# Kernel optimization log

Hardware: AMD Instinct MI355X
Metric: run time of the kernel (lower is better)

## Reference

```python
import jax, jax.numpy as jnp
import numpy as np

N_NODES = 20000
DEG = 32
N_EDGES = N_NODES * DEG
NUM_USERS = 100000
D = 128


def setup_inputs() -> dict:
    key = jax.random.key(0)
    ks = jax.random.split(key, 10)
    nodes = jax.random.randint(ks[0], (N_NODES,), 0, NUM_USERS)
    neigh_idx = jax.random.randint(ks[1], (N_EDGES,), 0, NUM_USERS)
    # fixed-degree flattening of the ragged to_neighs lists: every node has DEG neighbors
    seg_ids = jnp.repeat(jnp.arange(N_NODES), DEG)
    u2e = jax.random.normal(ks[2], (NUM_USERS, D), dtype=jnp.float32)
    W1 = jax.random.normal(ks[3], (2 * D, D), dtype=jnp.float32) * 0.05
    b1 = jax.random.normal(ks[4], (D,), dtype=jnp.float32) * 0.05
    W2 = jax.random.normal(ks[5], (D, D), dtype=jnp.float32) * 0.05
    b2 = jax.random.normal(ks[6], (D,), dtype=jnp.float32) * 0.05
    w3 = jax.random.normal(ks[7], (D, 1), dtype=jnp.float32) * 0.05
    b3 = jax.random.normal(ks[8], (1,), dtype=jnp.float32) * 0.05
    return {"nodes": nodes, "neigh_idx": neigh_idx, "seg_ids": seg_ids,
            "u2e": u2e, "W1": W1, "b1": b1, "W2": W2, "b2": b2, "w3": w3, "b3": b3}


def reference(nodes, neigh_idx, seg_ids, u2e, W1, b1, W2, b2, w3, b3):
    n = nodes.shape[0]
    e_u = u2e[neigh_idx]                 # [E, D] neighbor embeddings
    u_rep = u2e[nodes][seg_ids]          # [E, D] center-node embedding repeated per neighbor
    x = jnp.concatenate([e_u, u_rep], axis=1)        # [E, 2D]
    h = jax.nn.relu(x @ W1 + b1)                      # [E, D]
    h = jax.nn.relu(h @ W2 + b2)                      # [E, D]
    s = (h @ w3 + b3)[:, 0]                           # [E] attention logits
    # segment softmax over each node's neighbor set
    smax = jax.ops.segment_max(s, seg_ids, num_segments=n)
    e = jnp.exp(s - smax[seg_ids])
    denom = jax.ops.segment_sum(e, seg_ids, num_segments=n)
    att = e / denom[seg_ids]                          # [E]
    # attention-weighted neighbor sum (e_u^T @ att per node)
    out = jax.ops.segment_sum(att[:, None] * e_u, seg_ids, num_segments=n)  # [N, D]
    return out
```

## Files before the change

kernel.cpp:

```cpp
#include <hip/hip_runtime.h>
#include <hip/hip_bf16.h>

#define DD 128
#define DEG 32

typedef __attribute__((ext_vector_type(8))) _Float16 half8;
typedef __attribute__((ext_vector_type(4))) float f32x4;

__device__ __forceinline__ unsigned pkh(float a, float b) {
    _Float16 ha = (_Float16)a, hb = (_Float16)b;
    return (unsigned)__builtin_bit_cast(unsigned short, ha)
         | ((unsigned)__builtin_bit_cast(unsigned short, hb) << 16);
}
__device__ __forceinline__ float h2f_lo(unsigned u) {
    return (float)__builtin_bit_cast(_Float16, (unsigned short)(u & 0xffff));
}
__device__ __forceinline__ float h2f_hi(unsigned u) {
    return (float)__builtin_bit_cast(_Float16, (unsigned short)(u >> 16));
}

__global__ __launch_bounds__(256) void k_prep(
    const float* __restrict__ W1, const float* __restrict__ W2,
    uint4* __restrict__ w1img, uint4* __restrict__ w2t)
{
    int t = blockIdx.x * 256 + threadIdx.x;
    if (t < 4096) {
        int l = t & 63, f = t >> 6, k4 = f & 3, nt = f >> 2;
        int n = nt * 16 + (l & 15), kb = k4 * 32 + ((l >> 4) & 3) * 8;
        float v[8];
        #pragma unroll
        for (int i = 0; i < 8; ++i) {
            int k = kb + i;
            v[i] = (n < DD) ? W1[k * DD + n] : W1[(DD + k) * DD + (n - DD)];
        }
        uint4 r;
        r.x = pkh(v[0], v[1]); r.y = pkh(v[2], v[3]);
        r.z = pkh(v[4], v[5]); r.w = pkh(v[6], v[7]);
        w1img[t] = r;
    } else if (t < 6144) {
        int q = t - 4096;
        int l = q & 63, f = q >> 6, k4 = f & 3, mt = f >> 2;
        int ch = mt * 16 + (l & 15), kb = k4 * 32 + ((l >> 4) & 3) * 8;
        float v[8];
        #pragma unroll
        for (int i = 0; i < 8; ++i) v[i] = W2[(kb + i) * DD + ch];
        uint4 r;
        r.x = pkh(v[0], v[1]); r.y = pkh(v[2], v[3]);
        r.z = pkh(v[4], v[5]); r.w = pkh(v[6], v[7]);
        w2t[q] = r;
    }
}

__global__ __launch_bounds__(256) void k_cast(
    const float4* __restrict__ u2e4, uint4* __restrict__ ub16v, int total8)
{
    int i = blockIdx.x * 256 + threadIdx.x;
    if (i >= total8) return;
    float4 v0 = u2e4[(size_t)i * 2], v1 = u2e4[(size_t)i * 2 + 1];
    uint4 r;
    r.x = pkh(v0.x, v0.y); r.y = pkh(v0.z, v0.w);
    r.z = pkh(v1.x, v1.y); r.w = pkh(v1.z, v1.w);
    ub16v[i] = r;
}

__global__ __launch_bounds__(256) void k_qn(
    const int* __restrict__ nodes, const float* __restrict__ u2e,
    const uint4* __restrict__ w1img, const float* __restrict__ b1,
    unsigned short* __restrict__ Qnh, int n)
{
    const int t = threadIdx.x, w = t >> 6, l = t & 63;
    const int base = blockIdx.x * 128;

    half8 a[2][4];
    #pragma unroll
    for (int nt = 0; nt < 2; ++nt) {
        int row = min(base + w * 32 + nt * 16 + (l & 15), n - 1);
        int user = nodes[row];
        const float* rp = u2e + (size_t)user * DD + ((l >> 4) << 3);
        #pragma unroll
        for (int k4 = 0; k4 < 4; ++k4) {
            float4 v0 = *reinterpret_cast<const float4*>(rp + k4 * 32);
            float4 v1 = *reinterpret_cast<const float4*>(rp + k4 * 32 + 4);
            uint4 r;
            r.x = pkh(v0.x, v0.y); r.y = pkh(v0.z, v0.w);
            r.z = pkh(v1.x, v1.y); r.w = pkh(v1.z, v1.w);
            a[nt][k4] = __builtin_bit_cast(half8, r);
        }
    }
    const int chq = (l >> 4) << 2;
    #pragma unroll
    for (int mt = 0; mt < 8; ++mt) {
        half8 wf[4];
        #pragma unroll
        for (int k4 = 0; k4 < 4; ++k4)
            wf[k4] = __builtin_bit_cast(half8, w1img[((8 + mt) * 4 + k4) * 64 + l]);
        float4 b1v = *reinterpret_cast<const float4*>(&b1[mt * 16 + chq]);
        #pragma unroll
        for (int nt = 0; nt < 2; ++nt) {
            f32x4 acc = {0.f, 0.f, 0.f, 0.f};
            #pragma unroll
            for (int k4 = 0; k4 < 4; ++k4)
                acc = __builtin_amdgcn_mfma_f32_16x16x32_f16(wf[k4], a[nt][k4], acc, 0, 0, 0);
            int row = base + w * 32 + nt * 16 + (l & 15);
            if (row < n) {
                uint2 pk;
                pk.x = pkh(acc[0] + b1v.x, acc[1] + b1v.y);
                pk.y = pkh(acc[2] + b1v.z, acc[3] + b1v.w);
                *reinterpret_cast<uint2*>(&Qnh[(size_t)row * DD + mt * 16 + chq]) = pk;
            }
        }
    }
}

__global__ __launch_bounds__(512, 4) void k_node(
    const int* __restrict__ neigh, const _Float16* __restrict__ ub16,
    const unsigned short* __restrict__ Qnh, const uint4* __restrict__ w1img,
    const uint4* __restrict__ w2t, const float* __restrict__ b2,
    const float* __restrict__ w3, float4* __restrict__ out4, int n)
{
    __shared__ uint4 s_img[4096];

    const int t = threadIdx.x, w = t >> 6, l = t & 63;
    const int node = min(blockIdx.x * 8 + w, n - 1);
    const int g = l >> 4, c = l & 15;

    #pragma unroll
    for (int i = 0; i < 4; ++i) s_img[i * 512 + t] = w1img[i * 512 + t];
    #pragma unroll
    for (int i = 0; i < 4; ++i) s_img[2048 + i * 512 + t] = w2t[i * 512 + t];

    const int idx0 = neigh[node * DEG + c];
    const int idx1 = neigh[node * DEG + 16 + c];
    const int koff = g * 8;
    half8 ub0[4], ub1[4];
    #pragma unroll
    for (int k4 = 0; k4 < 4; ++k4)
        ub0[k4] = *reinterpret_cast<const half8*>(&ub16[(size_t)idx0 * DD + k4 * 32 + koff]);
    #pragma unroll
    for (int k4 = 0; k4 < 4; ++k4)
        ub1[k4] = *reinterpret_cast<const half8*>(&ub16[(size_t)idx1 * DD + k4 * 32 + koff]);
    uint2 qnh[8];
    #pragma unroll
    for (int mt = 0; mt < 8; ++mt)
        qnh[mt] = *reinterpret_cast<const uint2*>(&Qnh[(size_t)node * DD + mt * 16 + g * 4]);

    __syncthreads();

    uint2 hp0[8], hp1[8];
    #pragma unroll
    for (int mt = 0; mt < 8; ++mt) {
        half8 wf[4];
        #pragma unroll
        for (int k4 = 0; k4 < 4; ++k4)
            wf[k4] = __builtin_bit_cast(half8, s_img[(mt * 4 + k4) * 64 + l]);
        f32x4 a0 = {0.f, 0.f, 0.f, 0.f}, a1 = {0.f, 0.f, 0.f, 0.f};
        #pragma unroll
        for (int k4 = 0; k4 < 4; ++k4)
            a0 = __builtin_amdgcn_mfma_f32_16x16x32_f16(wf[k4], ub0[k4], a0, 0, 0, 0);
        #pragma unroll
        for (int k4 = 0; k4 < 4; ++k4)
            a1 = __builtin_amdgcn_mfma_f32_16x16x32_f16(wf[k4], ub1[k4], a1, 0, 0, 0);
        float q0 = h2f_lo(qnh[mt].x), q1 = h2f_hi(qnh[mt].x);
        float q2 = h2f_lo(qnh[mt].y), q3 = h2f_hi(qnh[mt].y);
        hp0[mt].x = pkh(fmaxf(a0[0] + q0, 0.f), fmaxf(a0[1] + q1, 0.f));
        hp0[mt].y = pkh(fmaxf(a0[2] + q2, 0.f), fmaxf(a0[3] + q3, 0.f));
        hp1[mt].x = pkh(fmaxf(a1[0] + q0, 0.f), fmaxf(a1[1] + q1, 0.f));
        hp1[mt].y = pkh(fmaxf(a1[2] + q2, 0.f), fmaxf(a1[3] + q3, 0.f));
    }

    const int srcA = ((g & 1) << 5) + c;
    const int hiSel = g >> 1;
    half8 hb0[4], hb1[4];
    #pragma unroll
    for (int k4 = 0; k4 < 4; ++k4) {
        unsigned d[4], e[4];
        #pragma unroll
        for (int j = 0; j < 4; ++j) {
            int src = srcA + ((j >> 1) << 4);
            unsigned vE = (unsigned)__shfl((int)((j & 1) ? hp0[2 * k4].y : hp0[2 * k4].x), src);
            unsigned vO = (unsigned)__shfl((int)((j & 1) ? hp0[2 * k4 + 1].y : hp0[2 * k4 + 1].x), src);
            d[j] = hiSel ? vO : vE;
            unsigned uE = (unsigned)__shfl((int)((j & 1) ? hp1[2 * k4].y : hp1[2 * k4].x), src);
            unsigned uO = (unsigned)__shfl((int)((j & 1) ? hp1[2 * k4 + 1].y : hp1[2 * k4 + 1].x), src);
            e[j] = hiSel ? uO : uE;
        }
        uint4 du = {d[0], d[1], d[2], d[3]};
        uint4 eu = {e[0], e[1], e[2], e[3]};
        hb0[k4] = __builtin_bit_cast(half8, du);
        hb1[k4] = __builtin_bit_cast(half8, eu);
    }

    float pl0 = 0.f, pl1 = 0.f;
    #pragma unroll
    for (int mt = 0; mt < 8; ++mt) {
        half8 wf[4];
        #pragma unroll
        for (int k4 = 0; k4 < 4; ++k4)
            wf[k4] = __builtin_bit_cast(half8, s_img[2048 + (mt * 4 + k4) * 64 + l]);
        float4 b2v = *reinterpret_cast<const float4*>(&b2[mt * 16 + g * 4]);
        float4 w3v = *reinterpret_cast<const float4*>(&w3[mt * 16 + g * 4]);
        f32x4 a0 = {0.f, 0.f, 0.f, 0.f}, a1 = {0.f, 0.f, 0.f, 0.f};
        #pragma unroll
        for (int k4 = 0; k4 < 4; ++k4)
            a0 = __builtin_amdgcn_mfma_f32_16x16x32_f16(wf[k4], hb0[k4], a0, 0, 0, 0);
        #pragma unroll
        for (int k4 = 0; k4 < 4; ++k4)
            a1 = __builtin_amdgcn_mfma_f32_16x16x32_f16(wf[k4], hb1[k4], a1, 0, 0, 0);
        pl0 += fmaxf(a0[0] + b2v.x, 0.f) * w3v.x + fmaxf(a0[1] + b2v.y, 0.f) * w3v.y
             + fmaxf(a0[2] + b2v.z, 0.f) * w3v.z + fmaxf(a0[3] + b2v.w, 0.f) * w3v.w;
        pl1 += fmaxf(a1[0] + b2v.x, 0.f) * w3v.x + fmaxf(a1[1] + b2v.y, 0.f) * w3v.y
             + fmaxf(a1[2] + b2v.z, 0.f) * w3v.z + fmaxf(a1[3] + b2v.w, 0.f) * w3v.w;
    }
    pl0 += __shfl_xor(pl0, 16); pl0 += __shfl_xor(pl0, 32);
    pl1 += __shfl_xor(pl1, 16); pl1 += __shfl_xor(pl1, 32);

    float mx = fmaxf(pl0, pl1);
    #pragma unroll
    for (int mask = 1; mask <= 8; mask <<= 1) mx = fmaxf(mx, __shfl_xor(mx, mask));
    float e0 = __expf(pl0 - mx), e1 = __expf(pl1 - mx);
    float sm = e0 + e1;
    #pragma unroll
    for (int mask = 1; mask <= 8; mask <<= 1) sm += __shfl_xor(sm, mask);
    float inv = __frcp_rn(sm);
    float att0 = e0 * inv, att1 = e1 * inv;

    float o[4][8];
    #pragma unroll
    for (int k4 = 0; k4 < 4; ++k4)
        #pragma unroll
        for (int i = 0; i < 8; ++i)
            o[k4][i] = att0 * (float)ub0[k4][i] + att1 * (float)ub1[k4][i];
    #pragma unroll
    for (int mask = 1; mask <= 8; mask <<= 1) {
        #pragma unroll
        for (int k4 = 0; k4 < 4; ++k4)
            #pragma unroll
            for (int i = 0; i < 8; ++i)
                o[k4][i] += __shfl_xor(o[k4][i], mask);
    }
    if (c == 0) {
        #pragma unroll
        for (int k4 = 0; k4 < 4; ++k4) {
            float4 r0 = make_float4(o[k4][0], o[k4][1], o[k4][2], o[k4][3]);
            float4 r1 = make_float4(o[k4][4], o[k4][5], o[k4][6], o[k4][7]);
            out4[(size_t)node * 32 + k4 * 8 + g * 2]     = r0;
            out4[(size_t)node * 32 + k4 * 8 + g * 2 + 1] = r1;
        }
    }
}

extern "C" void kernel_launch(void* const* d_in, const int* in_sizes, int n_in,
                              void* d_out, int out_size, void* d_ws, size_t ws_size,
                              hipStream_t stream)
{
    const int*   nodes = (const int*)  d_in[0];
    const int*   neigh = (const int*)  d_in[1];
    const float* u2e   = (const float*)d_in[3];
    const float* W1    = (const float*)d_in[4];
    const float* b1    = (const float*)d_in[5];
    const float* W2    = (const float*)d_in[6];
    const float* b2    = (const float*)d_in[7];
    const float* w3    = (const float*)d_in[8];

    const int n = in_sizes[0];
    const int U = in_sizes[3] / DD;

    uint4*          w1img = (uint4*)d_ws;
    uint4*          w2t   = w1img + 4096;
    _Float16*       ub16  = (_Float16*)(w2t + 2048);
    unsigned short* Qnh   = (unsigned short*)(ub16 + (size_t)U * DD);

    const int total8 = U * (DD / 8);

    k_prep<<<24, 256, 0, stream>>>(W1, W2, w1img, w2t);
    k_cast<<<(total8 + 255) / 256, 256, 0, stream>>>(
        (const float4*)u2e, (uint4*)ub16, total8);
    k_qn<<<(n + 127) / 128, 256, 0, stream>>>(nodes, u2e, w1img, b1, Qnh, n);
    k_node<<<(n + 7) / 8, 512, 0, stream>>>(neigh, ub16, Qnh, w1img, w2t,
                                            b2, w3, (float4*)d_out, n);
}
```

Before: 108.3 us.

## Read MLP weight fragments from global memory instead of LDS staging, merge prep kernels

The per-block 64KB LDS staging of the W1/W2 fragment images and its __syncthreads are removed from k_node. Each wave now reads its MFMA weight fragments directly from global memory, relying on L1/L2 caching. Blocks shrink to 256 threads (4 nodes) with a higher occupancy hint, since LDS no longer limits residency. The weight-prep and u2e-cast kernels are merged into one launch to save a launch. The cost is repeated global/L2 fragment loads per wave inside the MLP loops, in place of LDS reads.

```diff
diff --git a/kernel.cpp b/kernel.cpp
--- a/kernel.cpp
+++ b/kernel.cpp
@@ -19,48 +19,49 @@
     return (float)__builtin_bit_cast(_Float16, (unsigned short)(u >> 16));
 }
 
-__global__ __launch_bounds__(256) void k_prep(
+__global__ __launch_bounds__(256) void k_aux(
     const float* __restrict__ W1, const float* __restrict__ W2,
-    uint4* __restrict__ w1img, uint4* __restrict__ w2t)
-{
-    int t = blockIdx.x * 256 + threadIdx.x;
-    if (t < 4096) {
-        int l = t & 63, f = t >> 6, k4 = f & 3, nt = f >> 2;
-        int n = nt * 16 + (l & 15), kb = k4 * 32 + ((l >> 4) & 3) * 8;
-        float v[8];
-        #pragma unroll
-        for (int i = 0; i < 8; ++i) {
-            int k = kb + i;
-            v[i] = (n < DD) ? W1[k * DD + n] : W1[(DD + k) * DD + (n - DD)];
-        }
-        uint4 r;
-        r.x = pkh(v[0], v[1]); r.y = pkh(v[2], v[3]);
-        r.z = pkh(v[4], v[5]); r.w = pkh(v[6], v[7]);
-        w1img[t] = r;
-    } else if (t < 6144) {
-        int q = t - 4096;
-        int l = q & 63, f = q >> 6, k4 = f & 3, mt = f >> 2;
-        int ch = mt * 16 + (l & 15), kb = k4 * 32 + ((l >> 4) & 3) * 8;
-        float v[8];
-        #pragma unroll
-        for (int i = 0; i < 8; ++i) v[i] = W2[(kb + i) * DD + ch];
-        uint4 r;
-        r.x = pkh(v[0], v[1]); r.y = pkh(v[2], v[3]);
-        r.z = pkh(v[4], v[5]); r.w = pkh(v[6], v[7]);
-        w2t[q] = r;
-    }
-}
-
-__global__ __launch_bounds__(256) void k_cast(
-    const float4* __restrict__ u2e4, uint4* __restrict__ ub16v, int total8)
-{
-    int i = blockIdx.x * 256 + threadIdx.x;
-    if (i >= total8) return;
-    float4 v0 = u2e4[(size_t)i * 2], v1 = u2e4[(size_t)i * 2 + 1];
-    uint4 r;
-    r.x = pkh(v0.x, v0.y); r.y = pkh(v0.z, v0.w);
-    r.z = pkh(v1.x, v1.y); r.w = pkh(v1.z, v1.w);
-    ub16v[i] = r;
+    const float4* __restrict__ u2e4, uint4* __restrict__ w1img,
+    uint4* __restrict__ w2t, uint4* __restrict__ ub16v, int total8)
+{
+    const int bid = blockIdx.x;
+    if (bid < 24) {
+        int t = bid * 256 + threadIdx.x;
+        if (t < 4096) {
+            int l = t & 63, f = t >> 6, k4 = f & 3, nt = f >> 2;
+            int n = nt * 16 + (l & 15), kb = k4 * 32 + ((l >> 4) & 3) * 8;
+            float v[8];
+            #pragma unroll
+            for (int i = 0; i < 8; ++i) {
+                int k = kb + i;
+                v[i] = (n < DD) ? W1[k * DD + n] : W1[(DD + k) * DD + (n - DD)];
+            }
+            uint4 r;
+            r.x = pkh(v[0], v[1]); r.y = pkh(v[2], v[3]);
+            r.z = pkh(v[4], v[5]); r.w = pkh(v[6], v[7]);
+            w1img[t] = r;
+        } else if (t < 6144) {
+            int q = t - 4096;
+            int l = q & 63, f = q >> 6, k4 = f & 3, mt = f >> 2;
+            int ch = mt * 16 + (l & 15), kb = k4 * 32 + ((l >> 4) & 3) * 8;
+            float v[8];
+            #pragma unroll
+            for (int i = 0; i < 8; ++i) v[i] = W2[(kb + i) * DD + ch];
+            uint4 r;
+            r.x = pkh(v[0], v[1]); r.y = pkh(v[2], v[3]);
+            r.z = pkh(v[4], v[5]); r.w = pkh(v[6], v[7]);
+            w2t[q] = r;
+        }
+    } else {
+        int i = (bid - 24) * 256 + threadIdx.x;
+        if (i < total8) {
+            float4 v0 = u2e4[(size_t)i * 2], v1 = u2e4[(size_t)i * 2 + 1];
+            uint4 r;
+            r.x = pkh(v0.x, v0.y); r.y = pkh(v0.z, v0.w);
+            r.z = pkh(v1.x, v1.y); r.w = pkh(v1.z, v1.w);
+            ub16v[i] = r;
+        }
+    }
 }
 
 __global__ __launch_bounds__(256) void k_qn(
@@ -112,22 +113,15 @@
     }
 }
 
-__global__ __launch_bounds__(512, 4) void k_node(
+__global__ __launch_bounds__(256, 6) void k_node(
     const int* __restrict__ neigh, const _Float16* __restrict__ ub16,
     const unsigned short* __restrict__ Qnh, const uint4* __restrict__ w1img,
     const uint4* __restrict__ w2t, const float* __restrict__ b2,
     const float* __restrict__ w3, float4* __restrict__ out4, int n)
 {
-    __shared__ uint4 s_img[4096];
-
     const int t = threadIdx.x, w = t >> 6, l = t & 63;
-    const int node = min(blockIdx.x * 8 + w, n - 1);
+    const int node = min(blockIdx.x * 4 + w, n - 1);
     const int g = l >> 4, c = l & 15;
-
-    #pragma unroll
-    for (int i = 0; i < 4; ++i) s_img[i * 512 + t] = w1img[i * 512 + t];
-    #pragma unroll
-    for (int i = 0; i < 4; ++i) s_img[2048 + i * 512 + t] = w2t[i * 512 + t];
 
     const int idx0 = neigh[node * DEG + c];
     const int idx1 = neigh[node * DEG + 16 + c];
@@ -144,15 +138,13 @@
     for (int mt = 0; mt < 8; ++mt)
         qnh[mt] = *reinterpret_cast<const uint2*>(&Qnh[(size_t)node * DD + mt * 16 + g * 4]);
 
-    __syncthreads();
-
     uint2 hp0[8], hp1[8];
     #pragma unroll
     for (int mt = 0; mt < 8; ++mt) {
         half8 wf[4];
         #pragma unroll
         for (int k4 = 0; k4 < 4; ++k4)
-            wf[k4] = __builtin_bit_cast(half8, s_img[(mt * 4 + k4) * 64 + l]);
+            wf[k4] = __builtin_bit_cast(half8, w1img[(mt * 4 + k4) * 64 + l]);
         f32x4 a0 = {0.f, 0.f, 0.f, 0.f}, a1 = {0.f, 0.f, 0.f, 0.f};
         #pragma unroll
         for (int k4 = 0; k4 < 4; ++k4)
@@ -196,7 +188,7 @@
         half8 wf[4];
         #pragma unroll
         for (int k4 = 0; k4 < 4; ++k4)
-            wf[k4] = __builtin_bit_cast(half8, s_img[2048 + (mt * 4 + k4) * 64 + l]);
+            wf[k4] = __builtin_bit_cast(half8, w2t[(mt * 4 + k4) * 64 + l]);
         float4 b2v = *reinterpret_cast<const float4*>(&b2[mt * 16 + g * 4]);
         float4 w3v = *reinterpret_cast<const float4*>(&w3[mt * 16 + g * 4]);
         f32x4 a0 = {0.f, 0.f, 0.f, 0.f}, a1 = {0.f, 0.f, 0.f, 0.f};
@@ -272,10 +264,9 @@
 
     const int total8 = U * (DD / 8);
 
-    k_prep<<<24, 256, 0, stream>>>(W1, W2, w1img, w2t);
-    k_cast<<<(total8 + 255) / 256, 256, 0, stream>>>(
-        (const float4*)u2e, (uint4*)ub16, total8);
+    k_aux<<<24 + (total8 + 255) / 256, 256, 0, stream>>>(
+        W1, W2, (const float4*)u2e, w1img, w2t, (uint4*)ub16, total8);
     k_qn<<<(n + 127) / 128, 256, 0, stream>>>(nodes, u2e, w1img, b1, Qnh, n);
-    k_node<<<(n + 7) / 8, 512, 0, stream>>>(neigh, ub16, Qnh, w1img, w2t,
+    k_node<<<(n + 3) / 4, 256, 0, stream>>>(neigh, ub16, Qnh, w1img, w2t,
                                             b2, w3, (float4*)d_out, n);
 }
```

Measured after the change: 197.9 us. +82.7%, slower.
